# Kernel tuning notes

Measured on AMD Instinct MI355X. Metric: run time of the kernel, lower is better.

Reference implementation:

```python
import jax, jax.numpy as jnp
import numpy as np
from jax import lax

B, C, H, W = 16, 128, 128, 128
K = 3
EPS = 1e-8


def setup_inputs() -> dict:
    key = jax.random.key(0)
    k1, k2, k3 = jax.random.split(key, 3)
    x = jax.random.normal(k1, (B, C, H, W), dtype=jnp.float32)
    style = jax.random.normal(k2, (B, C), dtype=jnp.float32)
    weight = jax.random.normal(k3, (C, C, K, K), dtype=jnp.float32)
    return {"x": x, "style": style, "weight": weight}


def reference(x, style, weight):
    b = x.shape[0]
    o, i, kh, kw = weight.shape
    h, w_sp = x.shape[2], x.shape[3]
    # style / ||style||_inf over channel dim (per-sample scalar)
    s = style / jnp.max(jnp.abs(style), axis=1, keepdims=True)          # (B, i)
    # weight * (1/sqrt(i*kh*kw)) / ||weight||_inf over (i,kh,kw) per out channel
    wmax = jnp.max(jnp.abs(weight), axis=(1, 2, 3), keepdims=True)      # (o,1,1,1)
    wn = weight * (1.0 / jnp.sqrt(jnp.float32(i * kh * kw)) / wmax)     # (o,i,kh,kw)
    # per-sample modulation over input channels
    wmod = wn[None] * s[:, None, :, None, None]                         # (B,o,i,kh,kw)
    # demodulation (coe reshaped to (i,1,1,1) in torch; valid since o==i)
    coe = lax.rsqrt(jnp.sum(jnp.square(wmod), axis=(2, 3, 4)) + EPS)    # (B,o)
    wmod = wmod * coe[:, :, None, None, None]
    # fused batched conv via grouped-conv trick (StyleGAN2-style)
    xr = x.reshape(1, b * i, h, w_sp)
    wr = wmod.reshape(b * o, i, kh, kw)
    out = lax.conv_general_dilated(
        xr, wr,
        window_strides=(1, 1),
        padding=[(1, 1), (1, 1)],
        feature_group_count=b,
        dimension_numbers=("NCHW", "OIHW", "NCHW"),
    )
    return out.reshape(b, o, h, w_sp)
```

## Files before the change

### kernel.cpp

```cpp
#include <hip/hip_runtime.h>
#include <hip/hip_bf16.h>


#define BATCH 16
#define CH    128
#define HW    128
#define WPITCH 1152

#define WS_WMAX 0
#define WS_SN   128
#define WS_AFAC 2176
#define WS_WT   4224
#define WFRAG_BYTE_OFF 606720
#define WFRAG_BYTES    4718592
#define WS_NEEDED      (WFRAG_BYTE_OFF + WFRAG_BYTES)

typedef short  s8v  __attribute__((ext_vector_type(8)));
typedef float  f4v  __attribute__((ext_vector_type(4)));

__device__ inline unsigned short f2bf(float f) {
    union { float f; unsigned int u; } v; v.f = f;
    unsigned int r = v.u + 0x7FFFu + ((v.u >> 16) & 1u);
    return (unsigned short)(r >> 16);
}

__global__ __launch_bounds__(256) void k0_transpose(const float* __restrict__ w,
                                                    float* __restrict__ ws) {
    int idx = blockIdx.x * 256 + threadIdx.x;
    if (idx < CH * WPITCH) {
        int kt = idx >> 7;
        int o  = idx & 127;
        ws[WS_WT + idx] = w[(size_t)o * WPITCH + kt];
    }
}

__global__ __launch_bounds__(256) void k1_norms(const float* __restrict__ style,
                                                const float* __restrict__ weight,
                                                float* __restrict__ ws) {
    __shared__ float red[4];
    const int bid = blockIdx.x;
    const int t = threadIdx.x;
    if (bid < 128) {
        const int o = bid;
        float m = 0.f;
        for (int idx = t; idx < WPITCH; idx += 256)
            m = fmaxf(m, fabsf(weight[(size_t)o * WPITCH + idx]));
        #pragma unroll
        for (int off = 32; off > 0; off >>= 1)
            m = fmaxf(m, __shfl_down(m, off, 64));
        if ((t & 63) == 0) red[t >> 6] = m;
        __syncthreads();
        if (t == 0)
            ws[WS_WMAX + o] = fmaxf(fmaxf(red[0], red[1]), fmaxf(red[2], red[3]));
    } else {
        const int b = bid - 128;
        float v = (t < CH) ? style[b * CH + t] : 0.f;
        float m = fabsf(v);
        #pragma unroll
        for (int off = 32; off > 0; off >>= 1)
            m = fmaxf(m, __shfl_down(m, off, 64));
        if ((t & 63) == 0) red[t >> 6] = m;
        __syncthreads();
        float smax = fmaxf(fmaxf(red[0], red[1]), fmaxf(red[2], red[3]));
        if (t < CH) ws[WS_SN + b * CH + t] = v / smax;
    }
}

__global__ __launch_bounds__(256) void k2_coe(const float* __restrict__ weight,
                                              float* __restrict__ ws) {
    const int o = blockIdx.x;
    const int b = blockIdx.y;
    const int t = threadIdx.x;
    const float* sn = ws + WS_SN + b * CH;
    float s = 0.f;
    for (int idx = t; idx < WPITCH; idx += 256) {
        int i = idx / 9;
        float v = weight[(size_t)o * WPITCH + idx] * sn[i];
        s += v * v;
    }
    #pragma unroll
    for (int off = 32; off > 0; off >>= 1) s += __shfl_down(s, off, 64);
    __shared__ float red[4];
    if ((t & 63) == 0) red[t >> 6] = s;
    __syncthreads();
    if (t == 0) {
        float S = red[0] + red[1] + red[2] + red[3];
        float wm = ws[WS_WMAX + o];
        float scale = 1.0f / (sqrtf(1152.0f) * wm);
        float coe = rsqrtf(scale * scale * S + 1e-8f);
        ws[WS_AFAC + b * CH + o] = scale * coe;
    }
}

__global__ __launch_bounds__(256) void k3_swz(const float* __restrict__ ws,
                                              unsigned short* __restrict__ wfrag) {
    int t = blockIdx.x * 256 + threadIdx.x;
    const int lane = t & 63;
    int f = t >> 6;
    const int mo = f & 7;  f >>= 3;
    const int ci = f & 3;  f >>= 2;
    const int kk = f % 9;
    const int b  = f / 9;
    const int o  = mo * 16 + (lane & 15);
    const int i0 = ci * 32 + (lane >> 4) * 8;
    const float af = ws[WS_AFAC + b * CH + o];
    union { unsigned short u[8]; uint4 v; } pk;
    #pragma unroll
    for (int j = 0; j < 8; ++j) {
        int i = i0 + j;
        float v = ws[WS_WT + (size_t)(i * 9 + kk) * 128 + o] * af * ws[WS_SN + b * CH + i];
        pk.u[j] = f2bf(v);
    }
    *(uint4*)(wfrag + (size_t)t * 8) = pk.v;
}

#define XROW 132
#define XIP  40

__global__ __launch_bounds__(256, 2) void k4_mfma(const float* __restrict__ x,
                                                  const unsigned short* __restrict__ wfrag,
                                                  float* __restrict__ out) {
    const int h0 = blockIdx.x * 2;
    const int b  = blockIdx.y;
    const int t  = threadIdx.x;
    const int lane = t & 63;
    const int w    = t >> 6;
    const int ohalf = w & 1;
    const int rsel  = w >> 1;
    const int ln15  = lane & 15;
    const int quad  = lane >> 4;

    __shared__ unsigned short xT[4 * XROW * XIP];

    f4v acc[4][8];
    #pragma unroll
    for (int mt = 0; mt < 4; ++mt)
        #pragma unroll
        for (int nt = 0; nt < 8; ++nt)
            acc[mt][nt] = (f4v){0.f, 0.f, 0.f, 0.f};

    #pragma unroll 1
    for (int ci = 0; ci < 4; ++ci) {
        const int ib = ci * 32;
        __syncthreads();

        #pragma unroll 1
        for (int idx = t; idx < 16 * 130; idx += 256) {
            int c  = idx % 130;
            int ri = idx / 130;
            int r   = ri & 3;
            int ibk = ri >> 2;
            int row = h0 - 1 + r;
            int col = c - 1;
            union { unsigned short u[8]; s8v v; } pk;
            if ((unsigned)row < 128u && (unsigned)col < 128u) {
                const float* xp = x + (((size_t)(b * CH + ib + ibk * 8)) * HW + row) * HW + col;
                #pragma unroll
                for (int j = 0; j < 8; ++j)
                    pk.u[j] = f2bf(xp[(size_t)j * HW * HW]);
            } else {
                #pragma unroll
                for (int j = 0; j < 8; ++j) pk.u[j] = 0;
            }
            *(s8v*)&xT[(r * XROW + c) * XIP + ibk * 8] = pk.v;
        }
        __syncthreads();

        #pragma unroll 1
        for (int ky = 0; ky < 3; ++ky) {
            const int r = rsel + ky;
            #pragma unroll 1
            for (int kx = 0; kx < 3; ++kx) {
                const int kk = ky * 3 + kx;
                s8v a[4];
                #pragma unroll
                for (int mt = 0; mt < 4; ++mt) {
                    int mo = ohalf * 4 + mt;
                    size_t off = ((size_t)(((b * 9 + kk) * 4 + ci) * 8 + mo) * 64 + lane) * 8;
                    a[mt] = *(const s8v*)(wfrag + off);
                }
                s8v bf[8];
                #pragma unroll
                for (int nt = 0; nt < 8; ++nt) {
                    int c = nt * 16 + ln15 + kx;
                    bf[nt] = *(const s8v*)&xT[(r * XROW + c) * XIP + quad * 8];
                }
                #pragma unroll
                for (int mt = 0; mt < 4; ++mt)
                    #pragma unroll
                    for (int nt = 0; nt < 8; ++nt)
                        acc[mt][nt] = __builtin_amdgcn_mfma_f32_16x16x32_bf16(
                            a[mt], bf[nt], acc[mt][nt], 0, 0, 0);
            }
        }
    }

    const int orow = h0 + rsel;
    #pragma unroll
    for (int mt = 0; mt < 4; ++mt) {
        int o = ohalf * 64 + mt * 16 + quad * 4;
        #pragma unroll
        for (int nt = 0; nt < 8; ++nt) {
            int xcol = nt * 16 + ln15;
            float* op = out + (((size_t)(b * CH + o)) * HW + orow) * HW + xcol;
            #pragma unroll
            for (int reg = 0; reg < 4; ++reg)
                op[(size_t)reg * HW * HW] = acc[mt][nt][reg];
        }
    }
}

#define TI    8
#define XPITCH 132
__global__ __launch_bounds__(256) void k3_conv(const float* __restrict__ x,
                                               const float* __restrict__ ws,
                                               float* __restrict__ out) {
    const int h = blockIdx.x;
    const int b = blockIdx.y;
    const int t = threadIdx.x;
    const int og = t >> 4;
    const int pg = t & 15;

    __shared__ float x_lds[TI * 3 * XPITCH];
    __shared__ float w_lds[TI * 9 * 128];
    __shared__ float Af_l[128];
    __shared__ float sn_l[128];

    if (t < 128) {
        Af_l[t] = ws[WS_AFAC + b * CH + t];
        sn_l[t] = ws[WS_SN + b * CH + t];
    }
    float acc[8][8];
    #pragma unroll
    for (int j = 0; j < 8; ++j)
        #pragma unroll
        for (int p = 0; p < 8; ++p) acc[j][p] = 0.f;

    const float4* wt4 = (const float4*)(ws + WS_WT);
    float4* w_lds4 = (float4*)w_lds;
    const float4* Af4 = (const float4*)Af_l;

    #pragma unroll 1
    for (int ci = 0; ci < CH / TI; ++ci) {
        const int ib = ci * TI;
        __syncthreads();
        for (int idx = t; idx < TI * 3 * 130; idx += 256) {
            int ti  = idx / 390;
            int rem = idx - ti * 390;
            int r   = rem / 130;
            int c   = rem - r * 130;
            int row = h + r - 1;
            int col = c - 1;
            float v = 0.f;
            if ((unsigned)row < 128u && (unsigned)col < 128u)
                v = x[(((size_t)b * CH + ib + ti) * HW + row) * HW + col];
            x_lds[(ti * 3 + r) * XPITCH + c] = v;
        }
        for (int idx = t; idx < TI * 9 * 32; idx += 256) {
            int kt = idx >> 5;
            int o4 = idx & 31;
            int ti = kt / 9;
            float4 wv = wt4[(size_t)ib * 9 * 32 + idx];
            float4 af = Af4[o4];
            float  s  = sn_l[ib + ti];
            float4 rr;
            rr.x = wv.x * af.x * s; rr.y = wv.y * af.y * s;
            rr.z = wv.z * af.z * s; rr.w = wv.w * af.w * s;
            w_lds4[idx] = rr;
        }
        __syncthreads();
        #pragma unroll 1
        for (int ti = 0; ti < TI; ++ti) {
            float xv[3][12];
            #pragma unroll
            for (int ky = 0; ky < 3; ++ky)
                #pragma unroll
                for (int q = 0; q < 3; ++q) {
                    float4 v = *(const float4*)&x_lds[(ti * 3 + ky) * XPITCH + pg * 8 + q * 4];
                    xv[ky][q*4+0] = v.x; xv[ky][q*4+1] = v.y;
                    xv[ky][q*4+2] = v.z; xv[ky][q*4+3] = v.w;
                }
            #pragma unroll
            for (int kk = 0; kk < 9; ++kk) {
                const int ky = kk / 3;
                const int kx = kk % 3;
                float wv[8];
                #pragma unroll
                for (int q = 0; q < 2; ++q) {
                    float4 v = *(const float4*)&w_lds[(ti * 9 + kk) * 128 + og * 8 + q * 4];
                    wv[q*4+0] = v.x; wv[q*4+1] = v.y; wv[q*4+2] = v.z; wv[q*4+3] = v.w;
                }
                #pragma unroll
                for (int j = 0; j < 8; ++j)
                    #pragma unroll
                    for (int p = 0; p < 8; ++p)
                        acc[j][p] = fmaf(wv[j], xv[ky][p + kx], acc[j][p]);
            }
        }
    }
    const size_t obase = ((size_t)b * CH) * (HW * HW) + (size_t)h * HW;
    #pragma unroll
    for (int j = 0; j < 8; ++j) {
        int o = og * 8 + j;
        float4 v0 = {acc[j][0], acc[j][1], acc[j][2], acc[j][3]};
        float4 v1 = {acc[j][4], acc[j][5], acc[j][6], acc[j][7]};
        *(float4*)&out[obase + (size_t)o * (HW * HW) + pg * 8]     = v0;
        *(float4*)&out[obase + (size_t)o * (HW * HW) + pg * 8 + 4] = v1;
    }
}

extern "C" void kernel_launch(void* const* d_in, const int* in_sizes, int n_in,
                              void* d_out, int out_size, void* d_ws, size_t ws_size,
                              hipStream_t stream) {
    const float* x      = (const float*)d_in[0];
    const float* style  = (const float*)d_in[1];
    const float* weight = (const float*)d_in[2];
    float* out = (float*)d_out;
    float* ws  = (float*)d_ws;

    k0_transpose<<<(CH * WPITCH + 255) / 256, 256, 0, stream>>>(weight, ws);
    k1_norms<<<144, 256, 0, stream>>>(style, weight, ws);
    k2_coe<<<dim3(CH, BATCH), 256, 0, stream>>>(weight, ws);

    if (ws_size >= (size_t)WS_NEEDED) {
        unsigned short* wfrag = (unsigned short*)((char*)d_ws + WFRAG_BYTE_OFF);
        k3_swz<<<1152, 256, 0, stream>>>(ws, wfrag);
        k4_mfma<<<dim3(HW / 2, BATCH), 256, 0, stream>>>(x, wfrag, out);
    } else {
        k3_conv<<<dim3(HW, BATCH), 256, 0, stream>>>(x, ws, out);
    }
}
```

Measured before the change: 312.9 us.

## Vectorize x staging, prefetch weight fragments, drop transpose kernel on MFMA path

The x tile staging is rewritten so each thread loads float2 pairs from a single fixed row, replacing the old modulo-indexed scalar loop. Halo columns are zeroed once up front instead of on every pass. The weight-fragment loads are software-pipelined one kernel tap ahead inside a flattened 9-tap loop. The swizzle kernel now reads the original weight directly, so the transpose launch only runs on the fallback path. The goal is lower staging and launch overhead, at the cost of more registers for the prefetched fragments and strided reads in the swizzle.

```diff
diff --git a/kernel.cpp b/kernel.cpp
--- a/kernel.cpp
+++ b/kernel.cpp
@@ -17,6 +17,7 @@
 
 typedef short  s8v  __attribute__((ext_vector_type(8)));
 typedef float  f4v  __attribute__((ext_vector_type(4)));
+typedef float  f2v  __attribute__((ext_vector_type(2)));
 
 __device__ inline unsigned short f2bf(float f) {
     union { float f; unsigned int u; } v; v.f = f;
@@ -93,6 +94,7 @@
 }
 
 __global__ __launch_bounds__(256) void k3_swz(const float* __restrict__ ws,
+                                              const float* __restrict__ weight,
                                               unsigned short* __restrict__ wfrag) {
     int t = blockIdx.x * 256 + threadIdx.x;
     const int lane = t & 63;
@@ -108,7 +110,7 @@
     #pragma unroll
     for (int j = 0; j < 8; ++j) {
         int i = i0 + j;
-        float v = ws[WS_WT + (size_t)(i * 9 + kk) * 128 + o] * af * ws[WS_SN + b * CH + i];
+        float v = weight[(size_t)o * WPITCH + i * 9 + kk] * af * ws[WS_SN + b * CH + i];
         pk.u[j] = f2bf(v);
     }
     *(uint4*)(wfrag + (size_t)t * 8) = pk.v;
@@ -132,66 +134,83 @@
 
     __shared__ unsigned short xT[4 * XROW * XIP];
 
+    if (t < 32) {
+        const int zr   = t & 3;
+        const int zibk = (t >> 2) & 3;
+        const int zc   = (t >> 4) ? 129 : 0;
+        *(s8v*)&xT[(zr * XROW + zc) * XIP + zibk * 8] = (s8v){0, 0, 0, 0, 0, 0, 0, 0};
+    }
+
     f4v acc[4][8];
     #pragma unroll
     for (int mt = 0; mt < 4; ++mt)
         #pragma unroll
         for (int nt = 0; nt < 8; ++nt)
             acc[mt][nt] = (f4v){0.f, 0.f, 0.f, 0.f};
+
+    const int  cp     = t & 63;
+    const int  sr     = w;
+    const int  srow   = h0 - 1 + sr;
+    const bool svalid = (unsigned)srow < 128u;
+    const int  srcl   = svalid ? srow : 0;
 
     #pragma unroll 1
     for (int ci = 0; ci < 4; ++ci) {
         const int ib = ci * 32;
         __syncthreads();
 
+        #pragma unroll
+        for (int it = 0; it < 4; ++it) {
+            const float* xp = x + (((size_t)(b * CH + ib + it * 8)) * HW + srcl) * HW + 2 * cp;
+            f2v d[8];
+            #pragma unroll
+            for (int j = 0; j < 8; ++j)
+                d[j] = *(const f2v*)(xp + (size_t)j * HW * HW);
+            union { unsigned short u[16]; s8v v[2]; } pk;
+            #pragma unroll
+            for (int j = 0; j < 8; ++j) {
+                pk.u[j]     = f2bf(svalid ? d[j].x : 0.f);
+                pk.u[8 + j] = f2bf(svalid ? d[j].y : 0.f);
+            }
+            *(s8v*)&xT[(sr * XROW + (2 * cp + 1)) * XIP + it * 8] = pk.v[0];
+            *(s8v*)&xT[(sr * XROW + (2 * cp + 2)) * XIP + it * 8] = pk.v[1];
+        }
+        __syncthreads();
+
+        s8v aN[4];
+        #pragma unroll
+        for (int mt = 0; mt < 4; ++mt) {
+            const int mo = ohalf * 4 + mt;
+            aN[mt] = *(const s8v*)(wfrag +
+                     ((size_t)(((b * 9 + 0) * 4 + ci) * 8 + mo) * 64 + lane) * 8);
+        }
         #pragma unroll 1
-        for (int idx = t; idx < 16 * 130; idx += 256) {
-            int c  = idx % 130;
-            int ri = idx / 130;
-            int r   = ri & 3;
-            int ibk = ri >> 2;
-            int row = h0 - 1 + r;
-            int col = c - 1;
-            union { unsigned short u[8]; s8v v; } pk;
-            if ((unsigned)row < 128u && (unsigned)col < 128u) {
-                const float* xp = x + (((size_t)(b * CH + ib + ibk * 8)) * HW + row) * HW + col;
+        for (int kk = 0; kk < 9; ++kk) {
+            s8v aC[4];
+            #pragma unroll
+            for (int mt = 0; mt < 4; ++mt) aC[mt] = aN[mt];
+            const int kn = (kk < 8) ? kk + 1 : 8;
+            #pragma unroll
+            for (int mt = 0; mt < 4; ++mt) {
+                const int mo = ohalf * 4 + mt;
+                aN[mt] = *(const s8v*)(wfrag +
+                         ((size_t)(((b * 9 + kn) * 4 + ci) * 8 + mo) * 64 + lane) * 8);
+            }
+            const int ky = kk / 3;
+            const int kx = kk - ky * 3;
+            const int r  = rsel + ky;
+            s8v bf[8];
+            #pragma unroll
+            for (int nt = 0; nt < 8; ++nt) {
+                const int c = nt * 16 + ln15 + kx;
+                bf[nt] = *(const s8v*)&xT[(r * XROW + c) * XIP + quad * 8];
+            }
+            #pragma unroll
+            for (int mt = 0; mt < 4; ++mt)
                 #pragma unroll
-                for (int j = 0; j < 8; ++j)
-                    pk.u[j] = f2bf(xp[(size_t)j * HW * HW]);
-            } else {
-                #pragma unroll
-                for (int j = 0; j < 8; ++j) pk.u[j] = 0;
-            }
-            *(s8v*)&xT[(r * XROW + c) * XIP + ibk * 8] = pk.v;
-        }
-        __syncthreads();
-
-        #pragma unroll 1
-        for (int ky = 0; ky < 3; ++ky) {
-            const int r = rsel + ky;
-            #pragma unroll 1
-            for (int kx = 0; kx < 3; ++kx) {
-                const int kk = ky * 3 + kx;
-                s8v a[4];
-                #pragma unroll
-                for (int mt = 0; mt < 4; ++mt) {
-                    int mo = ohalf * 4 + mt;
-                    size_t off = ((size_t)(((b * 9 + kk) * 4 + ci) * 8 + mo) * 64 + lane) * 8;
-                    a[mt] = *(const s8v*)(wfrag + off);
-                }
-                s8v bf[8];
-                #pragma unroll
-                for (int nt = 0; nt < 8; ++nt) {
-                    int c = nt * 16 + ln15 + kx;
-                    bf[nt] = *(const s8v*)&xT[(r * XROW + c) * XIP + quad * 8];
-                }
-                #pragma unroll
-                for (int mt = 0; mt < 4; ++mt)
-                    #pragma unroll
-                    for (int nt = 0; nt < 8; ++nt)
-                        acc[mt][nt] = __builtin_amdgcn_mfma_f32_16x16x32_bf16(
-                            a[mt], bf[nt], acc[mt][nt], 0, 0, 0);
-            }
+                for (int nt = 0; nt < 8; ++nt)
+                    acc[mt][nt] = __builtin_amdgcn_mfma_f32_16x16x32_bf16(
+                        aC[mt], bf[nt], acc[mt][nt], 0, 0, 0);
         }
     }
 
@@ -318,15 +337,15 @@
     float* out = (float*)d_out;
     float* ws  = (float*)d_ws;
 
-    k0_transpose<<<(CH * WPITCH + 255) / 256, 256, 0, stream>>>(weight, ws);
     k1_norms<<<144, 256, 0, stream>>>(style, weight, ws);
     k2_coe<<<dim3(CH, BATCH), 256, 0, stream>>>(weight, ws);
 
     if (ws_size >= (size_t)WS_NEEDED) {
         unsigned short* wfrag = (unsigned short*)((char*)d_ws + WFRAG_BYTE_OFF);
-        k3_swz<<<1152, 256, 0, stream>>>(ws, wfrag);
+        k3_swz<<<1152, 256, 0, stream>>>(ws, weight, wfrag);
         k4_mfma<<<dim3(HW / 2, BATCH), 256, 0, stream>>>(x, wfrag, out);
     } else {
+        k0_transpose<<<(CH * WPITCH + 255) / 256, 256, 0, stream>>>(weight, ws);
         k3_conv<<<dim3(HW, BATCH), 256, 0, stream>>>(x, ws, out);
     }
 }
```

Result: no change. 313.2 us (+0.1%).
